# Performance work log

Measured on AMD Instinct MI355X. Metric: run time of the kernel, lower is better.

Reference implementation:

```python
import jax, jax.numpy as jnp
import numpy as np

N = 50000          # total residues (nodes)
E = 800000         # contact edges, avg degree 16
F_IN = 1280        # ESM embedding dim
H = 256            # hidden
L = 4              # num_layers
B = 100            # proteins in batch
MAX_NODES = 500    # residues per protein (uniform -> static to_dense_batch shape)


def setup_inputs() -> dict:
    key = jax.random.key(0)
    ks = jax.random.split(key, 16)
    s = 0.02
    inp = {
        "seq": jax.random.randint(ks[0], (N,), 0, 26),
        "edge_index": jax.random.randint(ks[1], (2, E), 0, N),
        "esm_token": jax.random.normal(ks[2], (N, F_IN), jnp.float32),
        "batch": jnp.arange(N) // MAX_NODES,
        # lin0
        "lin0_W": jax.random.normal(ks[3], (F_IN, H), jnp.float32) * s,
        "lin0_b": jnp.zeros((H,), jnp.float32),
        # WeightConv1 per layer: lin1 (root), lin2 (neighbor), lin3 (mask head)
        "wc_W1": jax.random.normal(ks[4], (L, H, H), jnp.float32) * s,
        "wc_b1": jnp.zeros((L, H), jnp.float32),
        "wc_W2": jax.random.normal(ks[5], (L, H, H), jnp.float32) * s,
        "wc_b2": jnp.zeros((L, H), jnp.float32),
        "wc_W3": jax.random.normal(ks[6], (L, H, H), jnp.float32) * s,
        "wc_b3": jnp.zeros((L, H), jnp.float32),
        # SparseConv per layer: neighbor weight + bias, root weight
        "sc_Wn": jax.random.normal(ks[7], (L, H, H), jnp.float32) * s,
        "sc_bn": jnp.zeros((L, H), jnp.float32),
        "sc_Wr": jax.random.normal(ks[8], (L, H, H), jnp.float32) * s,
    }
    return inp


def reference(seq, edge_index, esm_token, batch,
              lin0_W, lin0_b,
              wc_W1, wc_b1, wc_W2, wc_b2, wc_W3, wc_b3,
              sc_Wn, sc_bn, sc_Wr):
    src, dst = edge_index[0], edge_index[1]
    x = esm_token @ lin0_W + lin0_b              # [N, H]
    mask_val = None
    xs = []
    for i in range(L):
        # ---- WeightConv1: learned edge-conditioned node mask ----
        xm = x if mask_val is None else x * mask_val
        h_nb = xm @ wc_W2[i] + wc_b2[i]          # neighbor transform [N, H]
        agg = jax.ops.segment_sum(h_nb[src], dst, num_segments=N)
        h = jax.nn.relu(agg + xm @ wc_W1[i] + wc_b1[i])
        mask_val = jax.nn.sigmoid(h @ wc_W3[i] + wc_b3[i])   # [N, H]
        # ---- SparseConv: mask-gated sparse aggregation ----
        xg = x * mask_val
        agg2 = jax.ops.segment_sum(xg[src], dst, num_segments=N)
        x = jax.nn.relu(agg2 @ sc_Wn[i] + sc_bn[i] + x @ sc_Wr[i])
        xs.append(x)
    feat = jnp.concatenate(xs, axis=-1)          # jumping-knowledge cat [N, L*H]
    # ---- to_dense_batch ----
    counts = jax.ops.segment_sum(jnp.ones((N,), jnp.int32), batch, num_segments=B)
    starts = jnp.cumsum(counts) - counts
    pos = jnp.arange(N) - starts[batch]
    dense = jnp.zeros((B, MAX_NODES, L * H), feat.dtype).at[batch, pos].set(feat)
    node_mask = jnp.zeros((B, MAX_NODES), bool).at[batch, pos].set(True)
    return dense, node_mask
```

## Files before the change

### kernel.cpp

```cpp
#include <hip/hip_runtime.h>

#define NNODES 50000
#define HDIM 256
#define NLAYERS 4
#define NEDGES 800000
#define FIN 1280
#define LDOUT 1024

typedef _Float16 f16;
typedef __attribute__((ext_vector_type(8))) _Float16 f16x8;
typedef __attribute__((ext_vector_type(4))) _Float16 f16x4;
typedef __attribute__((ext_vector_type(4))) float f32x4;

enum { SRC_H = 0, SRC_CATH = 1 };
enum { EPI_HRELU = 0, EPI_MASKXG = 1, EPI_CATH2 = 2 };

template<int SRC, int EPI, int KTILES>
__global__ __launch_bounds__(256) void mgemm_k(
    const f16*  __restrict__ A3,
    const f16*  __restrict__ A4,
    const f16*  __restrict__ Xh,
    const int*  __restrict__ deg,
    const f16*  __restrict__ Wt,
    const float* __restrict__ bias,
    const float* __restrict__ bias2,
    float* __restrict__ Cf, int ldc,
    f16*  __restrict__ Ch,
    f16*  __restrict__ Ch2,
    f16*  __restrict__ Ch3)
{
    constexpr int K = KTILES * 64;
    __shared__ f16 Asm[2][4096];

    const int row0 = blockIdx.x * 64;
    const int tid = threadIdx.x;
    const int wv = tid >> 6;
    const int l = tid & 63;

    f32x4 acc[4][4] = {};

    const int sr = tid >> 2;
    const int sc0 = (tid & 3) * 16;
    const int grow = row0 + sr;
    const bool rok = grow < NNODES;
    const int lane_base0 =
        (((sc0 >> 5) * 4 + (sr >> 4)) * 64 + (sr & 15) + (((sc0 & 31) >> 3) * 16)) * 8;
    const int lane_base1 = lane_base0 + 128;

    const f16* bp[4];
    #pragma unroll
    for (int cf = 0; cf < 4; ++cf)
        bp[cf] = Wt + (size_t)(wv * 64 + cf * 16 + (l & 15)) * K + ((l >> 4) * 8);

    struct SReg { f16x8 h0, h1; };
    SReg RA, RB;

    auto LOAD = [&](SReg& r, int kt) {
        if (!rok) return;
        const int k0 = kt * 64 + sc0;
        const f16* p;
        if constexpr (SRC == SRC_CATH) {
            p = (k0 < HDIM) ? (A3 + (size_t)grow * HDIM + k0)
                            : (A4 + (size_t)grow * HDIM + (k0 - HDIM));
        } else {
            p = A3 + (size_t)grow * HDIM + k0;
        }
        r.h0 = *(const f16x8*)p;  r.h1 = *(const f16x8*)(p + 8);
    };

    auto COMMIT = [&](const SReg& r, int b) {
        f16x8 av0, av1;
        #pragma unroll
        for (int i = 0; i < 8; ++i) { av0[i] = (f16)0.f; av1[i] = (f16)0.f; }
        if (rok) { av0 = r.h0; av1 = r.h1; }
        *(f16x8*)(&Asm[b][lane_base0]) = av0;
        *(f16x8*)(&Asm[b][lane_base1]) = av1;
    };

    auto TILE = [&](int b, int kt) {
        f16x8 af[4][2];
        #pragma unroll
        for (int rf = 0; rf < 4; ++rf)
            #pragma unroll
            for (int kb = 0; kb < 2; ++kb)
                af[rf][kb] = *(const f16x8*)(&Asm[b][((kb * 4 + rf) * 64 + l) * 8]);
        f16x8 bfr[4][2];
        #pragma unroll
        for (int cf = 0; cf < 4; ++cf) {
            bfr[cf][0] = *(const f16x8*)(bp[cf] + kt * 64);
            bfr[cf][1] = *(const f16x8*)(bp[cf] + kt * 64 + 32);
        }
        #pragma unroll
        for (int cf = 0; cf < 4; ++cf)
            #pragma unroll
            for (int rf = 0; rf < 4; ++rf)
                #pragma unroll
                for (int kb = 0; kb < 2; ++kb)
                    acc[rf][cf] = __builtin_amdgcn_mfma_f32_16x16x32_f16(
                        af[rf][kb], bfr[cf][kb], acc[rf][cf], 0, 0, 0);
    };

    LOAD(RA, 0);
    COMMIT(RA, 0);
    if (KTILES > 1) LOAD(RB, 1);
    #pragma unroll
    for (int kt2 = 0; kt2 < KTILES; kt2 += 2) {
        __syncthreads();
        TILE(0, kt2);
        if (kt2 + 1 < KTILES) COMMIT(RB, 1);
        if (kt2 + 2 < KTILES) LOAD(RA, kt2 + 2);
        if (kt2 + 1 < KTILES) {
            __syncthreads();
            TILE(1, kt2 + 1);
            if (kt2 + 2 < KTILES) COMMIT(RA, 0);
            if (kt2 + 3 < KTILES) LOAD(RB, kt2 + 3);
        }
    }

    #pragma unroll
    for (int rf = 0; rf < 4; ++rf) {
        #pragma unroll
        for (int j = 0; j < 4; ++j) {
            const int row = row0 + rf * 16 + ((l >> 4) * 4) + j;
            if (row >= NNODES) continue;
            #pragma unroll
            for (int cf = 0; cf < 4; ++cf) {
                const int col = wv * 64 + cf * 16 + (l & 15);
                float v = acc[rf][cf][j];
                if constexpr (EPI == EPI_HRELU) {
                    const float dv = (float)deg[row];
                    v = fmaxf(v + dv * bias[col] + bias2[col], 0.f);
                    Ch[(size_t)row * HDIM + col] = (f16)v;
                } else if constexpr (EPI == EPI_MASKXG) {
                    const float m = 1.f / (1.f + expf(-(v + bias[col])));
                    Ch2[(size_t)row * HDIM + col] = (f16)m;
                    Ch[(size_t)row * HDIM + col] =
                        (f16)((float)Xh[(size_t)row * HDIM + col] * m);
                } else {
                    const float r = fmaxf(v + bias[col], 0.f);
                    Cf[(size_t)row * ldc + col] = r;
                    Ch[(size_t)row * HDIM + col] = (f16)r;
                    Ch3[(size_t)row * HDIM + col] =
                        (f16)(r * (float)Xh[(size_t)row * HDIM + col]);
                }
            }
        }
    }
}

template<int KTILES>
__global__ __launch_bounds__(256) void lin0_k(
    const float* __restrict__ A1, int lda1,
    const f16*  __restrict__ WtBase,
    f16* __restrict__ parts)
{
    constexpr int K = KTILES * 64;
    __shared__ f16 Asm[2][4096];

    const int row0 = blockIdx.x * 64;
    const int by = blockIdx.y;
    const int tid = threadIdx.x;
    const int wv = tid >> 6;
    const int l = tid & 63;

    f32x4 acc[4][4] = {};

    const int sr = tid >> 2;
    const int sc0 = (tid & 3) * 16;
    const int grow = row0 + sr;
    const bool rok = grow < NNODES;
    const int kg = by * K;
    const int lane_base0 =
        (((sc0 >> 5) * 4 + (sr >> 4)) * 64 + (sr & 15) + (((sc0 & 31) >> 3) * 16)) * 8;
    const int lane_base1 = lane_base0 + 128;

    const f16* Wsel = WtBase + (size_t)by * 256 * K;
    const f16* bp[4];
    #pragma unroll
    for (int cf = 0; cf < 4; ++cf)
        bp[cf] = Wsel + (size_t)(wv * 64 + cf * 16 + (l & 15)) * K + ((l >> 4) * 8);

    struct SReg { float4 f0, f1, f2, f3; };
    SReg RA, RB;

    auto LOAD = [&](SReg& r, int kt) {
        if (!rok) return;
        const float* p = A1 + (size_t)grow * lda1 + kg + kt * 64 + sc0;
        r.f0 = *(const float4*)(p + 0);  r.f1 = *(const float4*)(p + 4);
        r.f2 = *(const float4*)(p + 8);  r.f3 = *(const float4*)(p + 12);
    };

    auto COMMIT = [&](const SReg& r, int b) {
        f16x8 av0, av1;
        #pragma unroll
        for (int i = 0; i < 8; ++i) { av0[i] = (f16)0.f; av1[i] = (f16)0.f; }
        if (rok) {
            av0[0]=(f16)r.f0.x; av0[1]=(f16)r.f0.y; av0[2]=(f16)r.f0.z; av0[3]=(f16)r.f0.w;
            av0[4]=(f16)r.f1.x; av0[5]=(f16)r.f1.y; av0[6]=(f16)r.f1.z; av0[7]=(f16)r.f1.w;
            av1[0]=(f16)r.f2.x; av1[1]=(f16)r.f2.y; av1[2]=(f16)r.f2.z; av1[3]=(f16)r.f2.w;
            av1[4]=(f16)r.f3.x; av1[5]=(f16)r.f3.y; av1[6]=(f16)r.f3.z; av1[7]=(f16)r.f3.w;
        }
        *(f16x8*)(&Asm[b][lane_base0]) = av0;
        *(f16x8*)(&Asm[b][lane_base1]) = av1;
    };

    auto TILE = [&](int b, int kt) {
        f16x8 af[4][2];
        #pragma unroll
        for (int rf = 0; rf < 4; ++rf)
            #pragma unroll
            for (int kb = 0; kb < 2; ++kb)
                af[rf][kb] = *(const f16x8*)(&Asm[b][((kb * 4 + rf) * 64 + l) * 8]);
        f16x8 bfr[4][2];
        #pragma unroll
        for (int cf = 0; cf < 4; ++cf) {
            bfr[cf][0] = *(const f16x8*)(bp[cf] + kt * 64);
            bfr[cf][1] = *(const f16x8*)(bp[cf] + kt * 64 + 32);
        }
        #pragma unroll
        for (int cf = 0; cf < 4; ++cf)
            #pragma unroll
            for (int rf = 0; rf < 4; ++rf)
                #pragma unroll
                for (int kb = 0; kb < 2; ++kb)
                    acc[rf][cf] = __builtin_amdgcn_mfma_f32_16x16x32_f16(
                        af[rf][kb], bfr[cf][kb], acc[rf][cf], 0, 0, 0);
    };

    LOAD(RA, 0);
    COMMIT(RA, 0);
    if (KTILES > 1) LOAD(RB, 1);
    #pragma unroll
    for (int kt2 = 0; kt2 < KTILES; kt2 += 2) {
        __syncthreads();
        TILE(0, kt2);
        if (kt2 + 1 < KTILES) COMMIT(RB, 1);
        if (kt2 + 2 < KTILES) LOAD(RA, kt2 + 2);
        if (kt2 + 1 < KTILES) {
            __syncthreads();
            TILE(1, kt2 + 1);
            if (kt2 + 2 < KTILES) COMMIT(RA, 0);
            if (kt2 + 3 < KTILES) LOAD(RB, kt2 + 3);
        }
    }

    f16* Ph = parts + (size_t)by * NNODES * HDIM;
    #pragma unroll
    for (int rf = 0; rf < 4; ++rf) {
        #pragma unroll
        for (int j = 0; j < 4; ++j) {
            const int row = row0 + rf * 16 + ((l >> 4) * 4) + j;
            if (row >= NNODES) continue;
            #pragma unroll
            for (int cf = 0; cf < 4; ++cf) {
                const int col = wv * 64 + cf * 16 + (l & 15);
                Ph[(size_t)row * HDIM + col] = (f16)acc[rf][cf][j];
            }
        }
    }
}

__global__ __launch_bounds__(256) void combine4_k(
    const f16* __restrict__ parts, const float* __restrict__ b,
    f16* __restrict__ xh)
{
    const int t = blockIdx.x * 256 + threadIdx.x;
    const int row = t >> 6;
    const int c = (t & 63) * 4;
    if (row >= NNODES) return;
    const size_t NH = (size_t)NNODES * HDIM;
    const size_t off = (size_t)row * HDIM + c;
    f16x4 p0 = *(const f16x4*)(parts + off);
    f16x4 p1 = *(const f16x4*)(parts + NH + off);
    f16x4 p2 = *(const f16x4*)(parts + 2 * NH + off);
    f16x4 p3 = *(const f16x4*)(parts + 3 * NH + off);
    const float4 bb = *(const float4*)(b + c);
    f16x4 r;
    r[0] = (f16)((float)p0[0] + (float)p1[0] + (float)p2[0] + (float)p3[0] + bb.x);
    r[1] = (f16)((float)p0[1] + (float)p1[1] + (float)p2[1] + (float)p3[1] + bb.y);
    r[2] = (f16)((float)p0[2] + (float)p1[2] + (float)p2[2] + (float)p3[2] + bb.z);
    r[3] = (f16)((float)p0[3] + (float)p1[3] + (float)p2[3] + (float)p3[3] + bb.w);
    *(f16x4*)(xh + off) = r;
}

__global__ __launch_bounds__(256) void pack_all_k(
    const float* __restrict__ lin0_W,
    const float* __restrict__ W2, const float* __restrict__ W1,
    const float* __restrict__ W3,
    const float* __restrict__ Wn, const float* __restrict__ Wr,
    f16* __restrict__ dst)
{
    int idx = blockIdx.x * 256 + threadIdx.x;
    const int total = 327680 + 524288 + 262144 + 524288;
    if (idx >= total) return;
    f16* d = dst + idx;
    if (idx < 327680) {
        const int q = idx / 81920;
        int r = idx % 81920;
        const int col = r / 320, k = r % 320;
        *d = (f16)lin0_W[(size_t)(k + q * 320) * 256 + col];
        return;
    }
    idx -= 327680;
    if (idx < 524288) {
        const int i = idx / 131072;
        int r = idx % 131072;
        const int col = r / 512, k = r % 512;
        *d = (f16)(k < 256 ? W2[(size_t)i * 65536 + k * 256 + col]
                           : W1[(size_t)i * 65536 + (k - 256) * 256 + col]);
        return;
    }
    idx -= 524288;
    if (idx < 262144) {
        const int i = idx / 65536;
        int r = idx % 65536;
        const int col = r / 256, k = r % 256;
        *d = (f16)W3[(size_t)i * 65536 + k * 256 + col];
        return;
    }
    idx -= 262144;
    const int i = idx / 131072; int r = idx % 131072;
    const int col = r / 512, k = r % 512;
    *d = (f16)(k < 256 ? Wn[(size_t)i * 65536 + k * 256 + col]
                       : Wr[(size_t)i * 65536 + (k - 256) * 256 + col]);
}

__global__ __launch_bounds__(256) void count_k(
    const int* __restrict__ dstIdx, int* __restrict__ counts)
{
    const int e = blockIdx.x * 256 + threadIdx.x;
    if (e < NEDGES) atomicAdd(&counts[dstIdx[e]], 1);
}

__global__ __launch_bounds__(1024) void scan_k(
    const int* __restrict__ counts, int* __restrict__ starts)
{
    __shared__ int sm[1024];
    __shared__ int s_off;
    if (threadIdx.x == 0) s_off = 0;
    __syncthreads();
    for (int base = 0; base < NNODES; base += 1024) {
        const int i = base + threadIdx.x;
        const int v = (i < NNODES) ? counts[i] : 0;
        sm[threadIdx.x] = v;
        __syncthreads();
        for (int ofs = 1; ofs < 1024; ofs <<= 1) {
            const int t = (threadIdx.x >= ofs) ? sm[threadIdx.x - ofs] : 0;
            __syncthreads();
            sm[threadIdx.x] += t;
            __syncthreads();
        }
        const int incl = sm[threadIdx.x];
        const int off = s_off;
        if (i < NNODES) starts[i] = off + incl - v;
        __syncthreads();
        if (threadIdx.x == 1023) s_off = off + incl;
        __syncthreads();
    }
    if (threadIdx.x == 0) starts[NNODES] = s_off;
}

__global__ __launch_bounds__(256) void fillcsr_k(
    const int* __restrict__ srcIdx, const int* __restrict__ dstIdx,
    int* __restrict__ cursor, int* __restrict__ csr)
{
    const int e = blockIdx.x * 256 + threadIdx.x;
    if (e >= NEDGES) return;
    const int d = dstIdx[e];
    const int p = atomicAdd(&cursor[d], 1);
    csr[p] = srcIdx[e];
}

__global__ __launch_bounds__(256) void gather_g_k(
    const f16* __restrict__ rows, const int* __restrict__ csr,
    const int* __restrict__ starts, f16* __restrict__ outp)
{
    const int node = (blockIdx.x * 256 + threadIdx.x) >> 6;
    const int lane = threadIdx.x & 63;
    if (node >= NNODES) return;
    const int e0 = starts[node], e1 = starts[node + 1];
    float a0=0,a1=0,a2=0,a3=0, b0=0,b1=0,b2=0,b3=0;
    int e = e0;
    for (; e + 3 < e1; e += 4) {
        const int s0=csr[e], s1=csr[e+1], s2=csr[e+2], s3=csr[e+3];
        f16x4 v0 = *(const f16x4*)(rows + (size_t)s0 * HDIM + lane * 4);
        f16x4 v1 = *(const f16x4*)(rows + (size_t)s1 * HDIM + lane * 4);
        f16x4 v2 = *(const f16x4*)(rows + (size_t)s2 * HDIM + lane * 4);
        f16x4 v3 = *(const f16x4*)(rows + (size_t)s3 * HDIM + lane * 4);
        a0 += (float)v0[0] + (float)v2[0]; a1 += (float)v0[1] + (float)v2[1];
        a2 += (float)v0[2] + (float)v2[2]; a3 += (float)v0[3] + (float)v2[3];
        b0 += (float)v1[0] + (float)v3[0]; b1 += (float)v1[1] + (float)v3[1];
        b2 += (float)v1[2] + (float)v3[2]; b3 += (float)v1[3] + (float)v3[3];
    }
    for (; e < e1; ++e) {
        const int s0 = csr[e];
        f16x4 v0 = *(const f16x4*)(rows + (size_t)s0 * HDIM + lane * 4);
        a0 += (float)v0[0]; a1 += (float)v0[1]; a2 += (float)v0[2]; a3 += (float)v0[3];
    }
    f16x4 r;
    r[0] = (f16)(a0 + b0); r[1] = (f16)(a1 + b1);
    r[2] = (f16)(a2 + b2); r[3] = (f16)(a3 + b3);
    *(f16x4*)(outp + (size_t)node * HDIM + lane * 4) = r;
}

__global__ __launch_bounds__(256) void fill1_k(float* __restrict__ p, int n)
{
    const int t = blockIdx.x * 256 + threadIdx.x;
    if (t < n) p[t] = 1.0f;
}

extern "C" void kernel_launch(void* const* d_in, const int* in_sizes, int n_in,
                              void* d_out, int out_size, void* d_ws, size_t ws_size,
                              hipStream_t stream)
{
    const int*   edge   = (const int*)d_in[1];
    const int*   src    = edge;
    const int*   dst    = edge + NEDGES;
    const float* esm    = (const float*)d_in[2];
    const float* lin0_W = (const float*)d_in[4];
    const float* lin0_b = (const float*)d_in[5];
    const float* wc_W1  = (const float*)d_in[6];
    const float* wc_b1  = (const float*)d_in[7];
    const float* wc_W2  = (const float*)d_in[8];
    const float* wc_b2  = (const float*)d_in[9];
    const float* wc_W3  = (const float*)d_in[10];
    const float* wc_b3  = (const float*)d_in[11];
    const float* sc_Wn  = (const float*)d_in[12];
    const float* sc_bn  = (const float*)d_in[13];
    const float* sc_Wr  = (const float*)d_in[14];
    float* out = (float*)d_out;

    const size_t NH = (size_t)NNODES * HDIM;
    f16* parts = (f16*)d_ws;
    f16* aggx  = parts;
    f16* hbuf  = parts + NH;
    f16* xg    = parts + 2 * NH;
    f16* agg2  = parts + 3 * NH;
    f16* xh    = parts + 4 * NH;
    f16* xm    = xh + NH;
    f16* maskh = xm + NH;
    f16* wpack = maskh + NH;
    f16* lin0t = wpack;
    f16* WH    = lin0t + 327680;
    f16* W3t   = WH + 524288;
    f16* WtC   = W3t + 262144;
    int* iws    = (int*)(WtC + 524288);
    int* counts = iws;
    int* starts = iws + NNODES;
    int* cursor = iws + 2 * NNODES + 1;
    int* csr    = iws + 3 * NNODES + 2;

    const dim3 blk(256);
    const int gemmGrid = (NNODES + 63) / 64;
    const int edgeGrid = (NEDGES + 255) / 256;
    const int waveGrid = (NNODES * 64) / 256;

    hipMemsetAsync(counts, 0, NNODES * sizeof(int), stream);
    count_k<<<edgeGrid, blk, 0, stream>>>(dst, counts);
    scan_k<<<1, 1024, 0, stream>>>(counts, starts);
    hipMemcpyAsync(cursor, starts, NNODES * sizeof(int),
                   hipMemcpyDeviceToDevice, stream);
    fillcsr_k<<<edgeGrid, blk, 0, stream>>>(src, dst, cursor, csr);

    pack_all_k<<<(1638400 + 255) / 256, blk, 0, stream>>>(
        lin0_W, wc_W2, wc_W1, wc_W3, sc_Wn, sc_Wr, wpack);

    lin0_k<5><<<dim3(gemmGrid, 4), blk, 0, stream>>>(esm, FIN, lin0t, parts);
    combine4_k<<<waveGrid, blk, 0, stream>>>(parts, lin0_b, xh);

    for (int i = 0; i < NLAYERS; ++i) {
        const size_t bo = (size_t)i * HDIM;
        const f16* wh = WH + (size_t)i * 131072;
        const f16* w3 = W3t + (size_t)i * 65536;
        const f16* wc = WtC + (size_t)i * 131072;
        const f16* xmtab = (i == 0) ? xh : xm;

        gather_g_k<<<waveGrid, blk, 0, stream>>>(xmtab, csr, starts, aggx);
        mgemm_k<SRC_CATH, EPI_HRELU, 8><<<gemmGrid, blk, 0, stream>>>(
            aggx, xmtab, nullptr, counts, wh, wc_b2 + bo, wc_b1 + bo,
            nullptr, 0, hbuf, nullptr, nullptr);
        mgemm_k<SRC_H, EPI_MASKXG, 4><<<gemmGrid, blk, 0, stream>>>(
            hbuf, nullptr, xh, nullptr, w3, wc_b3 + bo, nullptr,
            nullptr, 0, xg, maskh, nullptr);
        gather_g_k<<<waveGrid, blk, 0, stream>>>(xg, csr, starts, agg2);
        mgemm_k<SRC_CATH, EPI_CATH2, 8><<<gemmGrid, blk, 0, stream>>>(
            agg2, xh, maskh, nullptr, wc, sc_bn + bo, nullptr,
            out + (size_t)i * HDIM, LDOUT, xh, nullptr, xm);
    }

    const size_t maskOff = (size_t)NNODES * LDOUT;
    fill1_k<<<(NNODES + 255) / 256, blk, 0, stream>>>(out + maskOff, NNODES);
}
```

Before: 1.353 ms.

## Fuse hidden-layer GEMM and mask-head GEMM into one kernel via LDS-resident h

Merges the WeightConv hidden GEMM (relu) and the mask-head GEMM (sigmoid, xg product) into a single kernel. The relu'd h tile is written into shared memory in MFMA fragment layout and consumed directly by the second GEMM, so the fp16 hbuf no longer makes a global round trip and one launch per layer goes away. In exchange, LDS usage grows to 32KB per block, which may lower occupancy, and the second GEMM's weight loads are software-prefetched in registers. The CATH2 GEMM is split out into its own specialized kernel with the same logic.

After: 1.312 ms. 1.03x faster.

```diff
diff --git a/kernel.cpp b/kernel.cpp
--- a/kernel.cpp
+++ b/kernel.cpp
@@ -12,25 +12,21 @@
 typedef __attribute__((ext_vector_type(4))) _Float16 f16x4;
 typedef __attribute__((ext_vector_type(4))) float f32x4;
 
-enum { SRC_H = 0, SRC_CATH = 1 };
-enum { EPI_HRELU = 0, EPI_MASKXG = 1, EPI_CATH2 = 2 };
-
-template<int SRC, int EPI, int KTILES>
-__global__ __launch_bounds__(256) void mgemm_k(
-    const f16*  __restrict__ A3,
-    const f16*  __restrict__ A4,
-    const f16*  __restrict__ Xh,
+
+__global__ __launch_bounds__(256) void hm_k(
+    const f16*  __restrict__ aggx,
+    const f16*  __restrict__ xm,
+    const f16*  __restrict__ xh,
     const int*  __restrict__ deg,
-    const f16*  __restrict__ Wt,
-    const float* __restrict__ bias,
-    const float* __restrict__ bias2,
-    float* __restrict__ Cf, int ldc,
-    f16*  __restrict__ Ch,
-    f16*  __restrict__ Ch2,
-    f16*  __restrict__ Ch3)
-{
-    constexpr int K = KTILES * 64;
-    __shared__ f16 Asm[2][4096];
+    const f16*  __restrict__ WH,
+    const f16*  __restrict__ W3t,
+    const float* __restrict__ b2,
+    const float* __restrict__ b1,
+    const float* __restrict__ b3,
+    f16* __restrict__ maskh,
+    f16* __restrict__ xg)
+{
+    __shared__ f16 lds[16384];
 
     const int row0 = blockIdx.x * 64;
     const int tid = threadIdx.x;
@@ -50,7 +46,7 @@
     const f16* bp[4];
     #pragma unroll
     for (int cf = 0; cf < 4; ++cf)
-        bp[cf] = Wt + (size_t)(wv * 64 + cf * 16 + (l & 15)) * K + ((l >> 4) * 8);
+        bp[cf] = WH + (size_t)(wv * 64 + cf * 16 + (l & 15)) * 512 + ((l >> 4) * 8);
 
     struct SReg { f16x8 h0, h1; };
     SReg RA, RB;
@@ -58,13 +54,8 @@
     auto LOAD = [&](SReg& r, int kt) {
         if (!rok) return;
         const int k0 = kt * 64 + sc0;
-        const f16* p;
-        if constexpr (SRC == SRC_CATH) {
-            p = (k0 < HDIM) ? (A3 + (size_t)grow * HDIM + k0)
-                            : (A4 + (size_t)grow * HDIM + (k0 - HDIM));
-        } else {
-            p = A3 + (size_t)grow * HDIM + k0;
-        }
+        const f16* p = (k0 < HDIM) ? (aggx + (size_t)grow * HDIM + k0)
+                                   : (xm + (size_t)grow * HDIM + (k0 - HDIM));
         r.h0 = *(const f16x8*)p;  r.h1 = *(const f16x8*)(p + 8);
     };
 
@@ -73,8 +64,8 @@
         #pragma unroll
         for (int i = 0; i < 8; ++i) { av0[i] = (f16)0.f; av1[i] = (f16)0.f; }
         if (rok) { av0 = r.h0; av1 = r.h1; }
-        *(f16x8*)(&Asm[b][lane_base0]) = av0;
-        *(f16x8*)(&Asm[b][lane_base1]) = av1;
+        *(f16x8*)(&lds[b * 4096 + lane_base0]) = av0;
+        *(f16x8*)(&lds[b * 4096 + lane_base1]) = av1;
     };
 
     auto TILE = [&](int b, int kt) {
@@ -83,7 +74,7 @@
         for (int rf = 0; rf < 4; ++rf)
             #pragma unroll
             for (int kb = 0; kb < 2; ++kb)
-                af[rf][kb] = *(const f16x8*)(&Asm[b][((kb * 4 + rf) * 64 + l) * 8]);
+                af[rf][kb] = *(const f16x8*)(&lds[b * 4096 + ((kb * 4 + rf) * 64 + l) * 8]);
         f16x8 bfr[4][2];
         #pragma unroll
         for (int cf = 0; cf < 4; ++cf) {
@@ -102,18 +93,80 @@
 
     LOAD(RA, 0);
     COMMIT(RA, 0);
-    if (KTILES > 1) LOAD(RB, 1);
-    #pragma unroll
-    for (int kt2 = 0; kt2 < KTILES; kt2 += 2) {
+    LOAD(RB, 1);
+    #pragma unroll
+    for (int kt2 = 0; kt2 < 8; kt2 += 2) {
         __syncthreads();
         TILE(0, kt2);
-        if (kt2 + 1 < KTILES) COMMIT(RB, 1);
-        if (kt2 + 2 < KTILES) LOAD(RA, kt2 + 2);
-        if (kt2 + 1 < KTILES) {
-            __syncthreads();
-            TILE(1, kt2 + 1);
-            if (kt2 + 2 < KTILES) COMMIT(RA, 0);
-            if (kt2 + 3 < KTILES) LOAD(RB, kt2 + 3);
+        COMMIT(RB, 1);
+        if (kt2 + 2 < 8) LOAD(RA, kt2 + 2);
+        __syncthreads();
+        TILE(1, kt2 + 1);
+        if (kt2 + 2 < 8) COMMIT(RA, 0);
+        if (kt2 + 3 < 8) LOAD(RB, kt2 + 3);
+    }
+    __syncthreads();
+
+    #pragma unroll
+    for (int rf = 0; rf < 4; ++rf) {
+        #pragma unroll
+        for (int j = 0; j < 4; ++j) {
+            const int rowl = rf * 16 + ((l >> 4) * 4) + j;
+            const int row = row0 + rowl;
+            const float dv = (row < NNODES) ? (float)deg[row] : 0.f;
+            #pragma unroll
+            for (int cf = 0; cf < 4; ++cf) {
+                const int col = wv * 64 + cf * 16 + (l & 15);
+                const float h = fmaxf(acc[rf][cf][j] + dv * b2[col] + b1[col], 0.f);
+                const int idx =
+                    (((col >> 6) * 8 + ((col >> 5) & 1) * 4 + (rowl >> 4)) * 64
+                     + ((col >> 3) & 3) * 16 + (rowl & 15)) * 8 + (col & 7);
+                lds[idx] = (f16)h;
+            }
+        }
+    }
+    __syncthreads();
+
+    const f16* bp3[4];
+    #pragma unroll
+    for (int cf = 0; cf < 4; ++cf)
+        bp3[cf] = W3t + (size_t)(wv * 64 + cf * 16 + (l & 15)) * 256 + ((l >> 4) * 8);
+
+    f32x4 acc2[4][4] = {};
+    f16x8 bC[4][2], bN[4][2];
+    #pragma unroll
+    for (int cf = 0; cf < 4; ++cf) {
+        bC[cf][0] = *(const f16x8*)(bp3[cf]);
+        bC[cf][1] = *(const f16x8*)(bp3[cf] + 32);
+    }
+    #pragma unroll
+    for (int kt = 0; kt < 4; ++kt) {
+        if (kt < 3) {
+            #pragma unroll
+            for (int cf = 0; cf < 4; ++cf) {
+                bN[cf][0] = *(const f16x8*)(bp3[cf] + (kt + 1) * 64);
+                bN[cf][1] = *(const f16x8*)(bp3[cf] + (kt + 1) * 64 + 32);
+            }
+        }
+        f16x8 af[4][2];
+        #pragma unroll
+        for (int rf = 0; rf < 4; ++rf)
+            #pragma unroll
+            for (int kb = 0; kb < 2; ++kb)
+                af[rf][kb] = *(const f16x8*)(&lds[((kt * 8 + kb * 4 + rf) * 64 + l) * 8]);
+        #pragma unroll
+        for (int cf = 0; cf < 4; ++cf)
+            #pragma unroll
+            for (int rf = 0; rf < 4; ++rf)
+                #pragma unroll
+                for (int kb = 0; kb < 2; ++kb)
+                    acc2[rf][cf] = __builtin_amdgcn_mfma_f32_16x16x32_f16(
+                        af[rf][kb], bC[cf][kb], acc2[rf][cf], 0, 0, 0);
+        if (kt < 3) {
+            #pragma unroll
+            for (int cf = 0; cf < 4; ++cf) {
+                bC[cf][0] = bN[cf][0];  bC[cf][1] = bN[cf][1];
+            }
         }
     }
 
@@ -126,23 +179,121 @@
             #pragma unroll
             for (int cf = 0; cf < 4; ++cf) {
                 const int col = wv * 64 + cf * 16 + (l & 15);
-                float v = acc[rf][cf][j];
-                if constexpr (EPI == EPI_HRELU) {
-                    const float dv = (float)deg[row];
-                    v = fmaxf(v + dv * bias[col] + bias2[col], 0.f);
-                    Ch[(size_t)row * HDIM + col] = (f16)v;
-                } else if constexpr (EPI == EPI_MASKXG) {
-                    const float m = 1.f / (1.f + expf(-(v + bias[col])));
-                    Ch2[(size_t)row * HDIM + col] = (f16)m;
-                    Ch[(size_t)row * HDIM + col] =
-                        (f16)((float)Xh[(size_t)row * HDIM + col] * m);
-                } else {
-                    const float r = fmaxf(v + bias[col], 0.f);
-                    Cf[(size_t)row * ldc + col] = r;
-                    Ch[(size_t)row * HDIM + col] = (f16)r;
-                    Ch3[(size_t)row * HDIM + col] =
-                        (f16)(r * (float)Xh[(size_t)row * HDIM + col]);
-                }
+                const float m = 1.f / (1.f + expf(-(acc2[rf][cf][j] + b3[col])));
+                maskh[(size_t)row * HDIM + col] = (f16)m;
+                xg[(size_t)row * HDIM + col] =
+                    (f16)((float)xh[(size_t)row * HDIM + col] * m);
+            }
+        }
+    }
+}
+
+__global__ __launch_bounds__(256) void cath2_k(
+    const f16*  __restrict__ A3,
+    const f16*  __restrict__ A4,
+    const f16*  __restrict__ Mh,
+    const f16*  __restrict__ Wt,
+    const float* __restrict__ bias,
+    float* __restrict__ Cf, int ldc,
+    f16*  __restrict__ Ch,
+    f16*  __restrict__ Ch3)
+{
+    constexpr int KTILES = 8;
+    constexpr int K = 512;
+    __shared__ f16 Asm[2][4096];
+
+    const int row0 = blockIdx.x * 64;
+    const int tid = threadIdx.x;
+    const int wv = tid >> 6;
+    const int l = tid & 63;
+
+    f32x4 acc[4][4] = {};
+
+    const int sr = tid >> 2;
+    const int sc0 = (tid & 3) * 16;
+    const int grow = row0 + sr;
+    const bool rok = grow < NNODES;
+    const int lane_base0 =
+        (((sc0 >> 5) * 4 + (sr >> 4)) * 64 + (sr & 15) + (((sc0 & 31) >> 3) * 16)) * 8;
+    const int lane_base1 = lane_base0 + 128;
+
+    const f16* bp[4];
+    #pragma unroll
+    for (int cf = 0; cf < 4; ++cf)
+        bp[cf] = Wt + (size_t)(wv * 64 + cf * 16 + (l & 15)) * K + ((l >> 4) * 8);
+
+    struct SReg { f16x8 h0, h1; };
+    SReg RA, RB;
+
+    auto LOAD = [&](SReg& r, int kt) {
+        if (!rok) return;
+        const int k0 = kt * 64 + sc0;
+        const f16* p = (k0 < HDIM) ? (A3 + (size_t)grow * HDIM + k0)
+                                   : (A4 + (size_t)grow * HDIM + (k0 - HDIM));
+        r.h0 = *(const f16x8*)p;  r.h1 = *(const f16x8*)(p + 8);
+    };
+
+    auto COMMIT = [&](const SReg& r, int b) {
+        f16x8 av0, av1;
+        #pragma unroll
+        for (int i = 0; i < 8; ++i) { av0[i] = (f16)0.f; av1[i] = (f16)0.f; }
+        if (rok) { av0 = r.h0; av1 = r.h1; }
+        *(f16x8*)(&Asm[b][lane_base0]) = av0;
+        *(f16x8*)(&Asm[b][lane_base1]) = av1;
+    };
+
+    auto TILE = [&](int b, int kt) {
+        f16x8 af[4][2];
+        #pragma unroll
+        for (int rf = 0; rf < 4; ++rf)
+            #pragma unroll
+            for (int kb = 0; kb < 2; ++kb)
+                af[rf][kb] = *(const f16x8*)(&Asm[b][((kb * 4 + rf) * 64 + l) * 8]);
+        f16x8 bfr[4][2];
+        #pragma unroll
+        for (int cf = 0; cf < 4; ++cf) {
+            bfr[cf][0] = *(const f16x8*)(bp[cf] + kt * 64);
+            bfr[cf][1] = *(const f16x8*)(bp[cf] + kt * 64 + 32);
+        }
+        #pragma unroll
+        for (int cf = 0; cf < 4; ++cf)
+            #pragma unroll
+            for (int rf = 0; rf < 4; ++rf)
+                #pragma unroll
+                for (int kb = 0; kb < 2; ++kb)
+                    acc[rf][cf] = __builtin_amdgcn_mfma_f32_16x16x32_f16(
+                        af[rf][kb], bfr[cf][kb], acc[rf][cf], 0, 0, 0);
+    };
+
+    LOAD(RA, 0);
+    COMMIT(RA, 0);
+    LOAD(RB, 1);
+    #pragma unroll
+    for (int kt2 = 0; kt2 < KTILES; kt2 += 2) {
+        __syncthreads();
+        TILE(0, kt2);
+        COMMIT(RB, 1);
+        if (kt2 + 2 < KTILES) LOAD(RA, kt2 + 2);
+        __syncthreads();
+        TILE(1, kt2 + 1);
+        if (kt2 + 2 < KTILES) COMMIT(RA, 0);
+        if (kt2 + 3 < KTILES) LOAD(RB, kt2 + 3);
+    }
+
+    #pragma unroll
+    for (int rf = 0; rf < 4; ++rf) {
+        #pragma unroll
+        for (int j = 0; j < 4; ++j) {
+            const int row = row0 + rf * 16 + ((l >> 4) * 4) + j;
+            if (row >= NNODES) continue;
+            #pragma unroll
+            for (int cf = 0; cf < 4; ++cf) {
+                const int col = wv * 64 + cf * 16 + (l & 15);
+                const float r = fmaxf(acc[rf][cf][j] + bias[col], 0.f);
+                Cf[(size_t)row * ldc + col] = r;
+                Ch[(size_t)row * HDIM + col] = (f16)r;
+                Ch3[(size_t)row * HDIM + col] =
+                    (f16)(r * (float)Mh[(size_t)row * HDIM + col]);
             }
         }
     }
@@ -433,9 +584,8 @@
     const size_t NH = (size_t)NNODES * HDIM;
     f16* parts = (f16*)d_ws;
     f16* aggx  = parts;
-    f16* hbuf  = parts + NH;
-    f16* xg    = parts + 2 * NH;
-    f16* agg2  = parts + 3 * NH;
+    f16* xg    = parts + NH;
+    f16* agg2  = parts + 2 * NH;
     f16* xh    = parts + 4 * NH;
     f16* xm    = xh + NH;
     f16* maskh = xm + NH;
@@ -476,16 +626,13 @@
         const f16* xmtab = (i == 0) ? xh : xm;
 
         gather_g_k<<<waveGrid, blk, 0, stream>>>(xmtab, csr, starts, aggx);
-        mgemm_k<SRC_CATH, EPI_HRELU, 8><<<gemmGrid, blk, 0, stream>>>(
-            aggx, xmtab, nullptr, counts, wh, wc_b2 + bo, wc_b1 + bo,
-            nullptr, 0, hbuf, nullptr, nullptr);
-        mgemm_k<SRC_H, EPI_MASKXG, 4><<<gemmGrid, blk, 0, stream>>>(
-            hbuf, nullptr, xh, nullptr, w3, wc_b3 + bo, nullptr,
-            nullptr, 0, xg, maskh, nullptr);
+        hm_k<<<gemmGrid, blk, 0, stream>>>(
+            aggx, xmtab, xh, counts, wh, w3,
+            wc_b2 + bo, wc_b1 + bo, wc_b3 + bo, maskh, xg);
         gather_g_k<<<waveGrid, blk, 0, stream>>>(xg, csr, starts, agg2);
-        mgemm_k<SRC_CATH, EPI_CATH2, 8><<<gemmGrid, blk, 0, stream>>>(
-            agg2, xh, maskh, nullptr, wc, sc_bn + bo, nullptr,
-            out + (size_t)i * HDIM, LDOUT, xh, nullptr, xm);
+        cath2_k<<<gemmGrid, blk, 0, stream>>>(
+            agg2, xh, maskh, wc, sc_bn + bo,
+            out + (size_t)i * HDIM, LDOUT, xh, xm);
     }
 
     const size_t maskOff = (size_t)NNODES * LDOUT;
```
